# Kernel tuning notes

Hardware: AMD Instinct MI355X
Metric: run time of the kernel (lower is better)

## Reference

```python
import jax, jax.numpy as jnp
import numpy as np

B, L = 1024, 1024
NCAT, NNUM = 20, 10
CAT_BUCKETS, SEQ_VOCAB = 100000, 50000
E, A, H, QH = 32, 128, 256, 256
TOPK = 30


def _init(key, shape, scale=0.02):
    return scale * jax.random.normal(key, shape, dtype=jnp.float32)


def setup_inputs() -> dict:
    key = jax.random.key(0)
    ks = jax.random.split(key, 24)
    z = lambda *s: jnp.zeros(s, dtype=jnp.float32)
    return {
        "cats": jax.random.randint(ks[0], (B, NCAT), 0, CAT_BUCKETS + 1),
        "nums": jax.random.normal(ks[1], (B, NNUM), dtype=jnp.float32),
        "seqs": jax.random.randint(ks[2], (B, L), 0, SEQ_VOCAB + 1),
        "tgt_ids": jax.random.randint(ks[3], (B,), 0, CAT_BUCKETS + 1),
        "cat_emb": _init(ks[4], (CAT_BUCKETS + 1, E)),
        "seq_emb": _init(ks[5], (SEQ_VOCAB + 1, E)),
        "Wnum": _init(ks[6], (NNUM, E)), "bnum": z(E),
        "Wq": _init(ks[7], (E, A)), "Wk": _init(ks[8], (E, A)), "Wv": _init(ks[9], (E, A)),
        "Wo": _init(ks[10], (A, E)), "bo": z(E),
        "Wpool": _init(ks[11], (NCAT * E, E)), "bpool": z(E),
        "Wmlp": _init(ks[12], (4 * E, H)), "bmlp": z(H),
        "q1_W1": _init(ks[13], (H, QH)), "q1_b1": z(QH),
        "q1_W2": _init(ks[14], (H, QH)), "q1_b2": z(QH),
        "q1_Wp": _init(ks[15], (QH, H)), "q1_bp": z(H),
        "q2_W1": _init(ks[16], (H, QH)), "q2_b1": z(QH),
        "q2_W2": _init(ks[17], (H, QH)), "q2_b2": z(QH),
        "q2_Wp": _init(ks[18], (QH, H)), "q2_bp": z(H),
        "Wout": _init(ks[19], (H, 1)), "bout": z(1),
    }


def _qnn(x, W1, b1, W2, b2, Wp, bp):
    # Quadratic neural block (QIN-style): Hadamard product of two linear maps,
    # projected back with a residual connection. Dropout is identity in eval.
    quad = (x @ W1 + b1) * (x @ W2 + b2)
    return x + quad @ Wp + bp


def reference(cats, nums, seqs, tgt_ids, cat_emb, seq_emb, Wnum, bnum, Wq, Wk, Wv,
              Wo, bo, Wpool, bpool, Wmlp, bmlp,
              q1_W1, q1_b1, q1_W2, q1_b2, q1_Wp, q1_bp,
              q2_W1, q2_b1, q2_W2, q2_b2, q2_Wp, q2_bp, Wout, bout):
    cat_e = cat_emb[cats]                                   # [B, NCAT, E]
    cat_pool = cat_e.reshape(cat_e.shape[0], -1) @ Wpool + bpool   # [B, E]
    num_e = nums @ Wnum + bnum                              # [B, E]
    tgt_e = cat_emb[tgt_ids]                                # [B, E] (tgt_emb shares cat_emb)
    seq_e = seq_emb[seqs]                                   # [B, L, E]

    q = tgt_e @ Wq                                          # [B, A]
    k = seq_e @ Wk                                          # [B, L, A]
    v = seq_e @ Wv                                          # [B, L, A]
    scores = jnp.einsum('ba,bla->bl', q, k) / jnp.sqrt(jnp.float32(A))

    # top-k + scatter mask + masked softmax == softmax over the top-k scores,
    # scattered implicitly via gather of the selected values.
    vals, idx = jax.lax.top_k(scores, TOPK)                 # [B, TOPK]
    w = jax.nn.softmax(vals, axis=1)                        # [B, TOPK]
    v_sel = jnp.take_along_axis(v, idx[:, :, None], axis=1)  # [B, TOPK, A]
    interest = jnp.einsum('bk,bka->ba', w, v_sel) @ Wo + bo  # [B, E]

    fused = jnp.concatenate([tgt_e, interest, cat_pool, num_e], axis=1)  # [B, 4E]
    h = jax.nn.relu(fused @ Wmlp + bmlp)                    # [B, H], dropout=eval
    h = _qnn(h, q1_W1, q1_b1, q1_W2, q1_b2, q1_Wp, q1_bp)
    h = _qnn(h, q2_W1, q2_b1, q2_W2, q2_b2, q2_Wp, q2_bp)
    return (h @ Wout + bout)[:, 0]                          # [B]
```

## Files before the change

kernel.cpp:

```cpp
#include <hip/hip_runtime.h>
#include <hip/hip_fp16.h>

#define B_ 1024
#define L_ 1024
#define NCAT_ 20
#define NNUM_ 10
#define E_ 32
#define A_ 128
#define H_ 256
#define TOPK_ 30
#define INV_SQRT_A 0.08838834764831845f

__device__ __forceinline__ void fma4(float4& a, float s, const float4 w) {
    a.x += s * w.x; a.y += s * w.y; a.z += s * w.z; a.w += s * w.w;
}
__device__ __forceinline__ float4 ldh4(const __half* p) {
    float2 rw = *(const float2*)p;
    const __half2* h = (const __half2*)&rw;
    float2 a = __half22float2(h[0]);
    float2 b = __half22float2(h[1]);
    return make_float4(a.x, a.y, b.x, b.y);
}
__device__ __forceinline__ void ldh24(const __half2* p, float4& w1, float4& w2) {
    float4 rw = *(const float4*)p;
    const __half2* h = (const __half2*)&rw;
    float2 f0 = __half22float2(h[0]), f1 = __half22float2(h[1]);
    float2 f2 = __half22float2(h[2]), f3 = __half22float2(h[3]);
    w1 = make_float4(f0.x, f1.x, f2.x, f3.x);
    w2 = make_float4(f0.y, f1.y, f2.y, f3.y);
}
__device__ __forceinline__ unsigned sortable(float f) {
    unsigned u = __float_as_uint(f);
    return (u & 0x80000000u) ? ~u : (u | 0x80000000u);
}
__device__ __forceinline__ float unsortable(unsigned s) {
    unsigned u = (s & 0x80000000u) ? (s ^ 0x80000000u) : ~s;
    return __uint_as_float(u);
}

#define K1_GRID 1356
__global__ __launch_bounds__(256) void fused_prep_kernel(
    const int* __restrict__ cats, const float* __restrict__ nums,
    const int* __restrict__ tgt_ids, const float* __restrict__ cat_emb,
    const float* __restrict__ Wnum, const float* __restrict__ bnum,
    const float* __restrict__ Wq, const float* __restrict__ Wk,
    const float* __restrict__ Wv, const float* __restrict__ Wo,
    const float* __restrict__ Wpool, const float* __restrict__ bpool,
    const float* __restrict__ seq_emb, const float* __restrict__ Wmlp,
    const float* __restrict__ q1W1, const float* __restrict__ q1W2,
    const float* __restrict__ q2W1, const float* __restrict__ q2W2,
    const float* __restrict__ q1Wp, const float* __restrict__ q2Wp,
    float* __restrict__ p_out, float* __restrict__ fused, float* __restrict__ M,
    __half2* __restrict__ seq_h2, __half2* __restrict__ Wmlp_h2,
    __half2* __restrict__ W12_1, __half2* __restrict__ W12_2,
    __half2* __restrict__ Wp1_h2, __half2* __restrict__ Wp2_h2)
{
    const int blk = blockIdx.x;
    const int t = threadIdx.x;

    if (blk < 256) {
        __shared__ float ce[4][NCAT_ * E_];
        __shared__ float tg[4][E_];
        __shared__ float nm[4][NNUM_];
        __shared__ float qs[4][A_];
        __shared__ float part[8][4][E_];
        const int r0 = blk * 4;

        for (int idx = t; idx < 640; idx += 256) {
            const int q = idx >> 3, f4 = idx & 7;
            const int row = q / 20, cat = q % 20;
            const int tok = cats[(r0 + row) * NCAT_ + cat];
            ((float4*)&ce[row][cat * 32])[f4] =
                ((const float4*)(cat_emb + (size_t)tok * 32))[f4];
        }
        if (t < 32) {
            const int row = t >> 3, f4 = t & 7;
            const int tok = tgt_ids[r0 + row];
            ((float4*)&tg[row][0])[f4] =
                ((const float4*)(cat_emb + (size_t)tok * 32))[f4];
        }
        if (t >= 64 && t < 104) {
            const int x = t - 64;
            nm[x / 10][x % 10] = nums[(r0 + x / 10) * NNUM_ + x % 10];
        }
        __syncthreads();

        {
            const int w = t >> 6, lane = t & 63;
            float q0 = 0.f, q1 = 0.f;
#pragma unroll
            for (int e = 0; e < E_; ++e) {
                float te = tg[w][e];
                q0 += te * Wq[e * A_ + lane];
                q1 += te * Wq[e * A_ + lane + 64];
            }
            qs[w][lane] = q0; qs[w][lane + 64] = q1;
        }

        {
            const int iseg = t >> 5;
            const int row = (t >> 3) & 3;
            const int c0 = (t & 7) * 4;
            float4 acc = make_float4(0.f, 0.f, 0.f, 0.f);
            const int i0 = iseg * 80;
            for (int i = i0; i < i0 + 80; ++i) {
                float4 wv = *(const float4*)(Wpool + i * 32 + c0);
                fma4(acc, ce[row][i], wv);
            }
            *(float4*)&part[iseg][row][c0] = acc;
        }
        __syncthreads();

        if (t < 128) {
            const int row = t >> 5, c = t & 31;
            const int b = r0 + row;
            float s = bpool[c];
#pragma unroll
            for (int g = 0; g < 8; ++g) s += part[g][row][c];
            fused[b * 128 + 64 + c] = s;
            fused[b * 128 + c] = tg[row][c];

            float ne = bnum[c];
#pragma unroll
            for (int n = 0; n < NNUM_; ++n) ne += nm[row][n] * Wnum[n * 32 + c];
            fused[b * 128 + 96 + c] = ne;

            float pv = 0.f;
#pragma unroll 8
            for (int a = 0; a < A_; ++a) pv += Wk[c * A_ + a] * qs[row][a];
            p_out[b * 32 + c] = pv;
        }
        return;
    }

    if (blk < 1280) {
        int x = (blk - 256) * 256 + t;
        for (; x < 800016; x += 1024 * 256) {
            float2 v = ((const float2*)seq_emb)[x];
            seq_h2[x] = __float22half2_rn(v);
        }
        return;
    }

    if (blk < 1284) {
        const int o = (blk - 1280) * 256 + t;
        const int j = o >> 5, e = o & 31;
        float sm = 0.f;
#pragma unroll 8
        for (int a = 0; a < A_; ++a) sm += Wv[j * A_ + a] * Wo[a * E_ + e];
        M[o] = sm;
        return;
    }

    if (blk < 1348) {
        int x = (blk - 1284) * 256 + t;
        for (; x < 65536; x += 64 * 256) {
            W12_1[x] = __float22half2_rn(make_float2(q1W1[x], q1W2[x]));
            W12_2[x] = __float22half2_rn(make_float2(q2W1[x], q2W2[x]));
        }
        return;
    }

    {
        int x = (blk - 1348) * 256 + t;
        for (; x < 16384; x += 8 * 256)
            Wmlp_h2[x] = __float22half2_rn(((const float2*)Wmlp)[x]);
        x = (blk - 1348) * 256 + t;
        for (; x < 32768; x += 8 * 256) {
            Wp1_h2[x] = __float22half2_rn(((const float2*)q1Wp)[x]);
            Wp2_h2[x] = __float22half2_rn(((const float2*)q2Wp)[x]);
        }
    }
}

#define RM 4
__global__ __launch_bounds__(512) void score_mlp_kernel(
    const int* __restrict__ seqs, const __half* __restrict__ seq_h,
    const float* __restrict__ seq_emb, const float* __restrict__ p,
    const float* __restrict__ M, const float* __restrict__ bo,
    const float* __restrict__ fused,
    const __half* __restrict__ Wmlp_h, const float* __restrict__ bmlp,
    const __half2* __restrict__ W12_1, const float* __restrict__ b11,
    const float* __restrict__ b12, const __half* __restrict__ Wp1_h,
    const float* __restrict__ b1p,
    const __half2* __restrict__ W12_2, const float* __restrict__ b21,
    const float* __restrict__ b22, const __half* __restrict__ Wp2_h,
    const float* __restrict__ b2p,
    const float* __restrict__ Wout, const float* __restrict__ bout,
    float* __restrict__ out)
{
    const int b0 = blockIdx.x * RM;
    const int tid = threadIdx.x;

    __shared__ float sc[RM][L_];
    __shared__ float ps[RM][E_];
    __shared__ float sw[RM][32];
    __shared__ int   stok[RM][32];
    __shared__ float xs[RM][128];
    __shared__ float hs[RM][H_];
    __shared__ float ts[RM][H_];
    __shared__ float part[8][RM][H_];
    __shared__ float red[8];

    if (tid < 128) ps[tid >> 5][tid & 31] = p[(b0 + (tid >> 5)) * 32 + (tid & 31)];
    __syncthreads();

    {
        const int row = tid >> 7;
        const int s = tid & 127;
        const int bb = b0 + row;
#pragma unroll
        for (int jj = 0; jj < 4; ++jj) {
            const int l1 = jj * 256 + s;
            const int l2 = l1 + 128;
            const int tok1 = seqs[bb * L_ + l1];
            const int tok2 = seqs[bb * L_ + l2];
            float4 buf[2][4];
            const float4* r1 = (const float4*)(seq_h + (size_t)tok1 * 32);
            const float4* r2 = (const float4*)(seq_h + (size_t)tok2 * 32);
#pragma unroll
            for (int i = 0; i < 4; ++i) buf[0][i] = r1[i];
#pragma unroll
            for (int i = 0; i < 4; ++i) buf[1][i] = r2[i];

            float acc0 = 0.f, acc1 = 0.f;
#pragma unroll
            for (int i = 0; i < 4; ++i) {
                const __half2* h1 = (const __half2*)&buf[0][i];
                const __half2* h2 = (const __half2*)&buf[1][i];
#pragma unroll
                for (int u = 0; u < 4; ++u) {
                    float2 f1 = __half22float2(h1[u]);
                    float2 f2 = __half22float2(h2[u]);
                    acc0 += f1.x * ps[row][i * 8 + 2 * u] + f1.y * ps[row][i * 8 + 2 * u + 1];
                    acc1 += f2.x * ps[row][i * 8 + 2 * u] + f2.y * ps[row][i * 8 + 2 * u + 1];
                }
            }
            sc[row][l1] = acc0 * INV_SQRT_A;
            sc[row][l2] = acc1 * INV_SQRT_A;
        }
    }
    if (tid < 384) {
        const int r = tid / 96, c0 = tid % 96;
        const int c = (c0 < 32) ? c0 : (c0 + 32);
        xs[r][c] = fused[(b0 + r) * 128 + c];
    }
    __syncthreads();

    if (tid < 256) {
        const int w = tid >> 6;
        const int lane = tid & 63;
        const int bb = b0 + w;

        unsigned long long key[16];
#pragma unroll
        for (int j = 0; j < 16; ++j) {
            const int l = j * 64 + lane;
            key[j] = ((unsigned long long)sortable(sc[w][l]) << 10)
                   | (unsigned)(1023 - l);
        }
#pragma unroll
        for (int a = 0; a < 15; ++a)
#pragma unroll
            for (int j = 0; j < 15 - a; ++j) {
                const bool swp = key[j] < key[j + 1];
                const unsigned long long hi = swp ? key[j + 1] : key[j];
                const unsigned long long lo = swp ? key[j] : key[j + 1];
                key[j] = hi; key[j + 1] = lo;
            }

        float myv = -1e30f; int myl = 0;
        unsigned long long front = key[0];
        for (int k = 0; k < TOPK_; ++k) {
            unsigned long long wk = front;
#pragma unroll
            for (int off = 32; off > 0; off >>= 1) {
                unsigned long long o = __shfl_xor(wk, off);
                if (o > wk) wk = o;
            }
            if (lane == k) {
                myv = unsortable((unsigned)(wk >> 10));
                myl = 1023 - (int)(wk & 1023);
            }
            if (front == wk) {
#pragma unroll
                for (int j = 0; j < 15; ++j) key[j] = key[j + 1];
                key[15] = 0ULL;
                front = key[0];
            }
        }

        float m = myv;
#pragma unroll
        for (int off = 32; off > 0; off >>= 1) m = fmaxf(m, __shfl_xor(m, off));
        float e = (lane < TOPK_) ? expf(myv - m) : 0.f;
        float s = e;
#pragma unroll
        for (int off = 32; off > 0; off >>= 1) s += __shfl_xor(s, off);
        if (lane < TOPK_) {
            sw[w][lane]   = e / s;
            stok[w][lane] = seqs[bb * L_ + myl];
        }

        if (lane < E_) {
            float acc = 0.f;
#pragma unroll
            for (int k = 0; k < TOPK_; ++k)
                acc += sw[w][k] * seq_emb[(size_t)stok[w][k] * 32 + lane];
            sc[w][lane] = acc;
        }
        if (lane < E_) {
            float acc = bo[lane];
#pragma unroll
            for (int j = 0; j < E_; ++j) acc += sc[w][j] * M[j * E_ + lane];
            xs[w][32 + lane] = acc;
        }
    }
    __syncthreads();

    const int cg = tid & 63;
    const int iseg = tid >> 6;
    const int c0 = cg * 4;

    {
        float4 acc[RM];
#pragma unroll
        for (int r = 0; r < RM; ++r) acc[r] = make_float4(0.f, 0.f, 0.f, 0.f);
        const int i0 = iseg * 16;
#pragma unroll
        for (int iq = 0; iq < 4; ++iq) {
            const int i = i0 + iq * 4;
            float4 w[4], xv[RM];
#pragma unroll
            for (int u = 0; u < 4; ++u) w[u] = ldh4(Wmlp_h + (i + u) * H_ + c0);
#pragma unroll
            for (int r = 0; r < RM; ++r) xv[r] = *(const float4*)(&xs[r][i]);
#pragma unroll
            for (int r = 0; r < RM; ++r) {
                fma4(acc[r], xv[r].x, w[0]); fma4(acc[r], xv[r].y, w[1]);
                fma4(acc[r], xv[r].z, w[2]); fma4(acc[r], xv[r].w, w[3]);
            }
        }
#pragma unroll
        for (int r = 0; r < RM; ++r) *(float4*)&part[iseg][r][c0] = acc[r];
    }
    __syncthreads();
    for (int o = tid; o < RM * H_; o += 512) {
        const int r = o >> 8, c = o & 255;
        float s = bmlp[c];
#pragma unroll
        for (int sg = 0; sg < 8; ++sg) s += part[sg][r][c];
        hs[r][c] = fmaxf(s, 0.f);
    }
    __syncthreads();

    const __half2* W12s[2] = { W12_1, W12_2 };
    const float* b1s[2] = { b11, b21 }; const float* b2s[2] = { b12, b22 };
    const __half* Wps[2] = { Wp1_h, Wp2_h }; const float* bps[2] = { b1p, b2p };

    for (int q = 0; q < 2; ++q) {
        const __half2* __restrict__ W12 = W12s[q];
        const __half*  __restrict__ Wp  = Wps[q];
        float4 a1[RM], a2[RM];
        {
#pragma unroll
            for (int r = 0; r < RM; ++r) {
                a1[r] = make_float4(0.f, 0.f, 0.f, 0.f);
                a2[r] = make_float4(0.f, 0.f, 0.f, 0.f);
            }
            const int i0 = iseg * 32;
#pragma unroll 2
            for (int iq = 0; iq < 8; ++iq) {
                const int i = i0 + iq * 4;
                float4 w1[4], w2[4], hv[RM];
#pragma unroll
                for (int u = 0; u < 4; ++u) ldh24(W12 + (i + u) * H_ + c0, w1[u], w2[u]);
#pragma unroll
                for (int r = 0; r < RM; ++r) hv[r] = *(const float4*)(&hs[r][i]);
#pragma unroll
                for (int r = 0; r < RM; ++r) {
                    fma4(a1[r], hv[r].x, w1[0]); fma4(a1[r], hv[r].y, w1[1]);
                    fma4(a1[r], hv[r].z, w1[2]); fma4(a1[r], hv[r].w, w1[3]);
                    fma4(a2[r], hv[r].x, w2[0]); fma4(a2[r], hv[r].y, w2[1]);
                    fma4(a2[r], hv[r].z, w2[2]); fma4(a2[r], hv[r].w, w2[3]);
                }
            }
        }
#pragma unroll
        for (int r = 0; r < RM; ++r) *(float4*)&part[iseg][r][c0] = a1[r];
        __syncthreads();
        {
            const float* b1 = b1s[q];
            for (int o = tid; o < RM * H_; o += 512) {
                const int r = o >> 8, c = o & 255;
                float t1 = b1[c];
#pragma unroll
                for (int sg = 0; sg < 8; ++sg) t1 += part[sg][r][c];
                ts[r][c] = t1;
            }
        }
        __syncthreads();
#pragma unroll
        for (int r = 0; r < RM; ++r) *(float4*)&part[iseg][r][c0] = a2[r];
        __syncthreads();
        {
            const float* b2 = b2s[q];
            for (int o = tid; o < RM * H_; o += 512) {
                const int r = o >> 8, c = o & 255;
                float t2 = b2[c];
#pragma unroll
                for (int sg = 0; sg < 8; ++sg) t2 += part[sg][r][c];
                ts[r][c] = ts[r][c] * t2;
            }
        }
        __syncthreads();

        {
            float4 ap[RM];
#pragma unroll
            for (int r = 0; r < RM; ++r) ap[r] = make_float4(0.f, 0.f, 0.f, 0.f);
            const int i0 = iseg * 32;
#pragma unroll 2
            for (int iq = 0; iq < 8; ++iq) {
                const int i = i0 + iq * 4;
                float4 w[4], tv[RM];
#pragma unroll
                for (int u = 0; u < 4; ++u) w[u] = ldh4(Wp + (i + u) * H_ + c0);
#pragma unroll
                for (int r = 0; r < RM; ++r) tv[r] = *(const float4*)(&ts[r][i]);
#pragma unroll
                for (int r = 0; r < RM; ++r) {
                    fma4(ap[r], tv[r].x, w[0]); fma4(ap[r], tv[r].y, w[1]);
                    fma4(ap[r], tv[r].z, w[2]); fma4(ap[r], tv[r].w, w[3]);
                }
            }
#pragma unroll
            for (int r = 0; r < RM; ++r) *(float4*)&part[iseg][r][c0] = ap[r];
        }
        __syncthreads();
        {
            const float* bp = bps[q];
            for (int o = tid; o < RM * H_; o += 512) {
                const int r = o >> 8, c = o & 255;
                float s = bp[c];
#pragma unroll
                for (int sg = 0; sg < 8; ++sg) s += part[sg][r][c];
                hs[r][c] += s;
            }
        }
        __syncthreads();
    }

    {
        const int r = tid >> 7, jj = tid & 127;
        float sum = hs[r][jj] * Wout[jj] + hs[r][jj + 128] * Wout[jj + 128];
#pragma unroll
        for (int off = 32; off > 0; off >>= 1) sum += __shfl_down(sum, off);
        if ((tid & 63) == 0) red[tid >> 6] = sum;
        __syncthreads();
        if (tid < RM) out[b0 + tid] = red[2 * tid] + red[2 * tid + 1] + bout[0];
    }
}

extern "C" void kernel_launch(void* const* d_in, const int* in_sizes, int n_in,
                              void* d_out, int out_size, void* d_ws, size_t ws_size,
                              hipStream_t stream) {
    const int*   cats    = (const int*)d_in[0];
    const float* nums    = (const float*)d_in[1];
    const int*   seqs    = (const int*)d_in[2];
    const int*   tgt_ids = (const int*)d_in[3];
    const float* cat_emb = (const float*)d_in[4];
    const float* seq_emb = (const float*)d_in[5];
    const float* Wnum    = (const float*)d_in[6];
    const float* bnum    = (const float*)d_in[7];
    const float* Wq      = (const float*)d_in[8];
    const float* Wk      = (const float*)d_in[9];
    const float* Wv      = (const float*)d_in[10];
    const float* Wo      = (const float*)d_in[11];
    const float* bo      = (const float*)d_in[12];
    const float* Wpool   = (const float*)d_in[13];
    const float* bpool   = (const float*)d_in[14];
    const float* Wmlp    = (const float*)d_in[15];
    const float* bmlp    = (const float*)d_in[16];
    const float* q1_W1   = (const float*)d_in[17];
    const float* q1_b1   = (const float*)d_in[18];
    const float* q1_W2   = (const float*)d_in[19];
    const float* q1_b2   = (const float*)d_in[20];
    const float* q1_Wp   = (const float*)d_in[21];
    const float* q1_bp   = (const float*)d_in[22];
    const float* q2_W1   = (const float*)d_in[23];
    const float* q2_b1   = (const float*)d_in[24];
    const float* q2_W2   = (const float*)d_in[25];
    const float* q2_b2   = (const float*)d_in[26];
    const float* q2_Wp   = (const float*)d_in[27];
    const float* q2_bp   = (const float*)d_in[28];
    const float* Wout    = (const float*)d_in[29];
    const float* bout    = (const float*)d_in[30];

    float* ws = (float*)d_ws;
    float*   p       = ws;
    float*   fused   = ws + 32768;
    float*   M       = ws + 163840;
    __half2* seq_h2  = (__half2*)(ws + 164864);
    __half2* Wmlp_h2 = (__half2*)(ws + 964928);
    __half2* W12_1   = (__half2*)(ws + 981312);
    __half2* W12_2   = (__half2*)(ws + 1046848);
    __half2* Wp1_h2  = (__half2*)(ws + 1112384);
    __half2* Wp2_h2  = (__half2*)(ws + 1145152);

    float* out = (float*)d_out;

    fused_prep_kernel<<<K1_GRID, 256, 0, stream>>>(
        cats, nums, tgt_ids, cat_emb, Wnum, bnum, Wq, Wk, Wv, Wo,
        Wpool, bpool, seq_emb, Wmlp,
        q1_W1, q1_W2, q2_W1, q2_W2, q1_Wp, q2_Wp,
        p, fused, M, seq_h2, Wmlp_h2, W12_1, W12_2, Wp1_h2, Wp2_h2);

    score_mlp_kernel<<<B_ / RM, 512, 0, stream>>>(
        seqs, (const __half*)seq_h2, seq_emb, p, M, bo, fused,
        (const __half*)Wmlp_h2, bmlp,
        W12_1, q1_b1, q1_b2, (const __half*)Wp1_h2, q1_bp,
        W12_2, q2_b1, q2_b2, (const __half*)Wp2_h2, q2_bp,
        Wout, bout, out);
}
```

Before: 179.4 us.

## Split score/top-k stage into per-row kernel separate from batched MLP kernel

The fused score+top-k+MLP kernel, which handled 4 batch rows per block, is split in two. A new kernel runs one block per batch row to compute scores, top-k, softmax and the interest vector, and writes the result into the fused buffer. A separate MLP kernel then reads the fused rows, 4 rows per block. This gives the gather-heavy scoring phase four times as many blocks and leaves fewer threads idle during top-k, at the cost of an extra kernel launch and a global round trip for the interest vector.

```diff
diff --git a/kernel.cpp b/kernel.cpp
--- a/kernel.cpp
+++ b/kernel.cpp
@@ -173,11 +173,122 @@
     }
 }
 
-#define RM 4
-__global__ __launch_bounds__(512) void score_mlp_kernel(
+__global__ __launch_bounds__(512) void score_topk_kernel(
     const int* __restrict__ seqs, const __half* __restrict__ seq_h,
     const float* __restrict__ seq_emb, const float* __restrict__ p,
     const float* __restrict__ M, const float* __restrict__ bo,
+    float* __restrict__ fused)
+{
+    const int b = blockIdx.x;
+    const int t = threadIdx.x;
+
+    __shared__ float sc[L_];
+    __shared__ float ps[E_];
+    __shared__ float sw[TOPK_];
+    __shared__ int   stok[TOPK_];
+
+    if (t < E_) ps[t] = p[b * E_ + t];
+    __syncthreads();
+
+    {
+        const int tok1 = seqs[b * L_ + t];
+        const int tok2 = seqs[b * L_ + t + 512];
+        float4 buf[2][4];
+        const float4* r1 = (const float4*)(seq_h + (size_t)tok1 * 32);
+        const float4* r2 = (const float4*)(seq_h + (size_t)tok2 * 32);
+#pragma unroll
+        for (int i = 0; i < 4; ++i) buf[0][i] = r1[i];
+#pragma unroll
+        for (int i = 0; i < 4; ++i) buf[1][i] = r2[i];
+
+        float acc0 = 0.f, acc1 = 0.f;
+#pragma unroll
+        for (int i = 0; i < 4; ++i) {
+            const __half2* h1 = (const __half2*)&buf[0][i];
+            const __half2* h2 = (const __half2*)&buf[1][i];
+#pragma unroll
+            for (int u = 0; u < 4; ++u) {
+                float2 f1 = __half22float2(h1[u]);
+                float2 f2 = __half22float2(h2[u]);
+                acc0 += f1.x * ps[i * 8 + 2 * u] + f1.y * ps[i * 8 + 2 * u + 1];
+                acc1 += f2.x * ps[i * 8 + 2 * u] + f2.y * ps[i * 8 + 2 * u + 1];
+            }
+        }
+        sc[t] = acc0 * INV_SQRT_A;
+        sc[t + 512] = acc1 * INV_SQRT_A;
+    }
+    __syncthreads();
+
+    if (t >= 64) return;
+    const int lane = t;
+
+    unsigned long long key[16];
+#pragma unroll
+    for (int j = 0; j < 16; ++j) {
+        const int l = j * 64 + lane;
+        key[j] = ((unsigned long long)sortable(sc[l]) << 10)
+               | (unsigned)(1023 - l);
+    }
+#pragma unroll
+    for (int a = 0; a < 15; ++a)
+#pragma unroll
+        for (int j = 0; j < 15 - a; ++j) {
+            const bool swp = key[j] < key[j + 1];
+            const unsigned long long hi = swp ? key[j + 1] : key[j];
+            const unsigned long long lo = swp ? key[j] : key[j + 1];
+            key[j] = hi; key[j + 1] = lo;
+        }
+
+    float myv = -1e30f; int myl = 0;
+    unsigned long long front = key[0];
+    for (int k = 0; k < TOPK_; ++k) {
+        unsigned long long wk = front;
+#pragma unroll
+        for (int off = 32; off > 0; off >>= 1) {
+            unsigned long long o = __shfl_xor(wk, off);
+            if (o > wk) wk = o;
+        }
+        if (lane == k) {
+            myv = unsortable((unsigned)(wk >> 10));
+            myl = 1023 - (int)(wk & 1023);
+        }
+        if (front == wk) {
+#pragma unroll
+            for (int j = 0; j < 15; ++j) key[j] = key[j + 1];
+            key[15] = 0ULL;
+            front = key[0];
+        }
+    }
+
+    float m = myv;
+#pragma unroll
+    for (int off = 32; off > 0; off >>= 1) m = fmaxf(m, __shfl_xor(m, off));
+    float e = (lane < TOPK_) ? expf(myv - m) : 0.f;
+    float s = e;
+#pragma unroll
+    for (int off = 32; off > 0; off >>= 1) s += __shfl_xor(s, off);
+    if (lane < TOPK_) {
+        sw[lane]   = e / s;
+        stok[lane] = seqs[b * L_ + myl];
+    }
+
+    if (lane < E_) {
+        float acc = 0.f;
+#pragma unroll
+        for (int k = 0; k < TOPK_; ++k)
+            acc += sw[k] * seq_emb[(size_t)stok[k] * 32 + lane];
+        sc[lane] = acc;
+    }
+    if (lane < E_) {
+        float acc = bo[lane];
+#pragma unroll
+        for (int j = 0; j < E_; ++j) acc += sc[j] * M[j * E_ + lane];
+        fused[b * 128 + 32 + lane] = acc;
+    }
+}
+
+#define RM 4
+__global__ __launch_bounds__(512) void mlp_kernel(
     const float* __restrict__ fused,
     const __half* __restrict__ Wmlp_h, const float* __restrict__ bmlp,
     const __half2* __restrict__ W12_1, const float* __restrict__ b11,
@@ -191,136 +302,18 @@
 {
     const int b0 = blockIdx.x * RM;
     const int tid = threadIdx.x;
-
-    __shared__ float sc[RM][L_];
-    __shared__ float ps[RM][E_];
-    __shared__ float sw[RM][32];
-    __shared__ int   stok[RM][32];
+    const int cg = tid & 63;
+    const int iseg = tid >> 6;
+    const int c0 = cg * 4;
+
     __shared__ float xs[RM][128];
     __shared__ float hs[RM][H_];
     __shared__ float ts[RM][H_];
     __shared__ float part[8][RM][H_];
     __shared__ float red[8];
 
-    if (tid < 128) ps[tid >> 5][tid & 31] = p[(b0 + (tid >> 5)) * 32 + (tid & 31)];
+    for (int i = tid; i < RM * 128; i += 512) xs[i >> 7][i & 127] = fused[b0 * 128 + i];
     __syncthreads();
-
-    {
-        const int row = tid >> 7;
-        const int s = tid & 127;
-        const int bb = b0 + row;
-#pragma unroll
-        for (int jj = 0; jj < 4; ++jj) {
-            const int l1 = jj * 256 + s;
-            const int l2 = l1 + 128;
-            const int tok1 = seqs[bb * L_ + l1];
-            const int tok2 = seqs[bb * L_ + l2];
-            float4 buf[2][4];
-            const float4* r1 = (const float4*)(seq_h + (size_t)tok1 * 32);
-            const float4* r2 = (const float4*)(seq_h + (size_t)tok2 * 32);
-#pragma unroll
-            for (int i = 0; i < 4; ++i) buf[0][i] = r1[i];
-#pragma unroll
-            for (int i = 0; i < 4; ++i) buf[1][i] = r2[i];
-
-            float acc0 = 0.f, acc1 = 0.f;
-#pragma unroll
-            for (int i = 0; i < 4; ++i) {
-                const __half2* h1 = (const __half2*)&buf[0][i];
-                const __half2* h2 = (const __half2*)&buf[1][i];
-#pragma unroll
-                for (int u = 0; u < 4; ++u) {
-                    float2 f1 = __half22float2(h1[u]);
-                    float2 f2 = __half22float2(h2[u]);
-                    acc0 += f1.x * ps[row][i * 8 + 2 * u] + f1.y * ps[row][i * 8 + 2 * u + 1];
-                    acc1 += f2.x * ps[row][i * 8 + 2 * u] + f2.y * ps[row][i * 8 + 2 * u + 1];
-                }
-            }
-            sc[row][l1] = acc0 * INV_SQRT_A;
-            sc[row][l2] = acc1 * INV_SQRT_A;
-        }
-    }
-    if (tid < 384) {
-        const int r = tid / 96, c0 = tid % 96;
-        const int c = (c0 < 32) ? c0 : (c0 + 32);
-        xs[r][c] = fused[(b0 + r) * 128 + c];
-    }
-    __syncthreads();
-
-    if (tid < 256) {
-        const int w = tid >> 6;
-        const int lane = tid & 63;
-        const int bb = b0 + w;
-
-        unsigned long long key[16];
-#pragma unroll
-        for (int j = 0; j < 16; ++j) {
-            const int l = j * 64 + lane;
-            key[j] = ((unsigned long long)sortable(sc[w][l]) << 10)
-                   | (unsigned)(1023 - l);
-        }
-#pragma unroll
-        for (int a = 0; a < 15; ++a)
-#pragma unroll
-            for (int j = 0; j < 15 - a; ++j) {
-                const bool swp = key[j] < key[j + 1];
-                const unsigned long long hi = swp ? key[j + 1] : key[j];
-                const unsigned long long lo = swp ? key[j] : key[j + 1];
-                key[j] = hi; key[j + 1] = lo;
-            }
-
-        float myv = -1e30f; int myl = 0;
-        unsigned long long front = key[0];
-        for (int k = 0; k < TOPK_; ++k) {
-            unsigned long long wk = front;
-#pragma unroll
-            for (int off = 32; off > 0; off >>= 1) {
-                unsigned long long o = __shfl_xor(wk, off);
-                if (o > wk) wk = o;
-            }
-            if (lane == k) {
-                myv = unsortable((unsigned)(wk >> 10));
-                myl = 1023 - (int)(wk & 1023);
-            }
-            if (front == wk) {
-#pragma unroll
-                for (int j = 0; j < 15; ++j) key[j] = key[j + 1];
-                key[15] = 0ULL;
-                front = key[0];
-            }
-        }
-
-        float m = myv;
-#pragma unroll
-        for (int off = 32; off > 0; off >>= 1) m = fmaxf(m, __shfl_xor(m, off));
-        float e = (lane < TOPK_) ? expf(myv - m) : 0.f;
-        float s = e;
-#pragma unroll
-        for (int off = 32; off > 0; off >>= 1) s += __shfl_xor(s, off);
-        if (lane < TOPK_) {
-            sw[w][lane]   = e / s;
-            stok[w][lane] = seqs[bb * L_ + myl];
-        }
-
-        if (lane < E_) {
-            float acc = 0.f;
-#pragma unroll
-            for (int k = 0; k < TOPK_; ++k)
-                acc += sw[w][k] * seq_emb[(size_t)stok[w][k] * 32 + lane];
-            sc[w][lane] = acc;
-        }
-        if (lane < E_) {
-            float acc = bo[lane];
-#pragma unroll
-            for (int j = 0; j < E_; ++j) acc += sc[w][j] * M[j * E_ + lane];
-            xs[w][32 + lane] = acc;
-        }
-    }
-    __syncthreads();
-
-    const int cg = tid & 63;
-    const int iseg = tid >> 6;
-    const int c0 = cg * 4;
 
     {
         float4 acc[RM];
@@ -516,9 +509,11 @@
         q1_W1, q1_W2, q2_W1, q2_W2, q1_Wp, q2_Wp,
         p, fused, M, seq_h2, Wmlp_h2, W12_1, W12_2, Wp1_h2, Wp2_h2);
 
-    score_mlp_kernel<<<B_ / RM, 512, 0, stream>>>(
-        seqs, (const __half*)seq_h2, seq_emb, p, M, bo, fused,
-        (const __half*)Wmlp_h2, bmlp,
+    score_topk_kernel<<<B_, 512, 0, stream>>>(
+        seqs, (const __half*)seq_h2, seq_emb, p, M, bo, fused);
+
+    mlp_kernel<<<B_ / RM, 512, 0, stream>>>(
+        fused, (const __half*)Wmlp_h2, bmlp,
         W12_1, q1_b1, q1_b2, (const __half*)Wp1_h2, q1_bp,
         W12_2, q2_b1, q2_b2, (const __half*)Wp2_h2, q2_bp,
         Wout, bout, out);
```

New measurement: 186.4 us. 1.04x slower.
